# Kernel tuning notes

Hardware: AMD Instinct MI355X
Metric: run time of the kernel (lower is better)

Reference implementation:

```python
import jax, jax.numpy as jnp
import numpy as np

# Architecture constants pinned by the source script
D_MODEL = 2      # input_size / problemDim
ED = 64          # d_inner = expand_factor * d_model = hidden_size
N = 32           # d_state
K = 16           # d_conv
DT_RANK = 1      # ceil(d_model / 16)
NC = 4           # num_classes
B, L = 16, 2048


def setup_inputs() -> dict:
    key = jax.random.key(0)
    ks = jax.random.split(key, 16)
    rn = lambda k, shape, sc=0.1: jax.random.normal(k, shape, jnp.float32) * sc
    return {
        "x": jax.random.normal(ks[0], (B, L, D_MODEL), jnp.float32),
        "norm_w": jnp.ones((D_MODEL,), jnp.float32),
        "w_in": rn(ks[1], (D_MODEL, 2 * ED)),            # in_proj (no bias)
        "conv_w": rn(ks[2], (ED, 1, K)),                  # depthwise causal conv
        "conv_b": rn(ks[3], (ED,)),
        "w_xproj": rn(ks[4], (ED, DT_RANK + 2 * N)),      # x_proj (no bias)
        "w_dt": rn(ks[5], (DT_RANK, ED)),                 # dt_proj
        "b_dt": rn(ks[6], (ED,)),
        "A_log": jnp.log(jnp.tile(jnp.arange(1, N + 1, dtype=jnp.float32), (ED, 1))),
        "D_skip": jnp.ones((ED,), jnp.float32),
        "w_out": rn(ks[7], (ED, ED)),                     # out_proj (classifier mode: d_inner->d_inner)
        "b_out": rn(ks[8], (ED,)),
        "w_fc": rn(ks[9], (ED, ED)),
        "b_fc": rn(ks[10], (ED,)),
        "w_cls": rn(ks[11], (ED, NC)),
        "b_cls": rn(ks[12], (NC,)),
        "w_reg": rn(ks[13], (ED, 1)),
        "b_reg": rn(ks[14], (1,)),
    }


def _rmsnorm(x, w, eps=1e-5):
    return x * jax.lax.rsqrt(jnp.mean(x * x, axis=-1, keepdims=True) + eps) * w


def _silu(x):
    return x * jax.nn.sigmoid(x)


def reference(x, norm_w, w_in, conv_w, conv_b, w_xproj, w_dt, b_dt, A_log, D_skip,
              w_out, b_out, w_fc, b_fc, w_cls, b_cls, w_reg, b_reg):
    # --- Mamba block (n_layers = 1, classifier mode: no residual back to d_model) ---
    h = _rmsnorm(x, norm_w)                                # [B,L,D]
    xz = h @ w_in                                          # [B,L,2*ED]
    xb, z = jnp.split(xz, 2, axis=-1)
    # depthwise causal conv over time (torch pads K-1 both sides then slices [:L] == left-pad K-1)
    xc = jnp.transpose(xb, (0, 2, 1))                      # [B,ED,L]
    xc = jax.lax.conv_general_dilated(
        xc, conv_w, window_strides=(1,), padding=[(K - 1, 0)],
        feature_group_count=ED, dimension_numbers=("NCH", "OIH", "NCH"))
    xc = xc + conv_b[None, :, None]
    xb = _silu(jnp.transpose(xc, (0, 2, 1)))               # [B,L,ED]
    # input-dependent SSM parameters
    dbc = xb @ w_xproj                                     # [B,L,dt_rank+2N]
    delta = jax.nn.softplus(dbc[..., :DT_RANK] @ w_dt + b_dt)   # [B,L,ED]
    Bm = dbc[..., DT_RANK:DT_RANK + N]                     # [B,L,N]
    C = dbc[..., DT_RANK + N:]                             # [B,L,N]
    A = -jnp.exp(A_log)                                    # [ED,N]
    dA = jnp.exp(delta[..., None] * A)                     # [B,L,ED,N]
    dBx = delta[..., None] * Bm[:, :, None, :] * xb[..., None]  # [B,L,ED,N]

    # selective scan: h_t = dA_t * h_{t-1} + dBx_t ; y_t = <h_t, C_t>
    def step(hst, inp):
        dA_t, dBx_t, C_t = inp
        hst = dA_t * hst + dBx_t                           # [B,ED,N]
        y = jnp.einsum("ben,bn->be", hst, C_t)
        return hst, y

    h0 = jnp.zeros((x.shape[0], ED, N), x.dtype)
    xs = (jnp.transpose(dA, (1, 0, 2, 3)),
          jnp.transpose(dBx, (1, 0, 2, 3)),
          jnp.transpose(C, (1, 0, 2)))
    _, ys = jax.lax.scan(step, h0, xs)                     # [L,B,ED]
    y = jnp.transpose(ys, (1, 0, 2)) + D_skip * xb         # [B,L,ED]
    y = y * _silu(z)                                       # gate
    out = y @ w_out + b_out                                # [B,L,ED]

    last = out[:, -1, :]                                   # [B,ED]
    hs = jax.nn.relu(last @ w_fc + b_fc)
    class_logits = hs @ w_cls + b_cls                      # [B,NC]
    mass_pred = (hs @ w_reg + b_reg)[:, 0]                 # [B]
    return class_logits, mass_pred
```

## Files before the change

kernel.cpp:

```cpp
#include <hip/hip_runtime.h>
#include <math.h>

#define BB 16
#define LL 2048
#define ED 64
#define NN 32
#define KK 16
#define NCHUNK 32
#define CH 64
#define NBLK (BB * NCHUNK)

struct ShB {
    float dl[CH][ED];
    float rl[CH][ED];
    float bml[CH][NN + 1];
    float dtr[CH];
};

__global__ __launch_bounds__(256) void k1_featscan(
    const float* __restrict__ x, const float* __restrict__ norm_w,
    const float* __restrict__ w_in, const float* __restrict__ conv_w,
    const float* __restrict__ conv_b, const float* __restrict__ w_xproj,
    const float* __restrict__ w_dt, const float* __restrict__ b_dt,
    const float* __restrict__ A_log,
    float* __restrict__ pbuf, float* __restrict__ sbuf,
    float* __restrict__ xlast, float* __restrict__ zl, float* __restrict__ cl)
{
    const int bx = blockIdx.x;
    const int b = bx >> 5, ti = bx & 31;
    const int l0 = ti * CH;
    const int tid = threadIdx.x;

    __shared__ float xbl[CH][ED + 1];
    __shared__ union { float pre[CH + KK - 1][ED]; ShB sb; } u;
    __shared__ float hh[2 * (CH + KK - 1)];

    if (tid < 2 * (CH + KK - 1)) {
        int p = tid >> 1, c = tid & 1;
        int l = l0 - (KK - 1) + p;
        hh[tid] = (l >= 0) ? x[(b * LL + l) * 2 + c] : 0.f;
    }
    __syncthreads();
    if (tid < CH + KK - 1) {
        float x0 = hh[2 * tid], x1 = hh[2 * tid + 1];
        float s = rsqrtf(0.5f * (x0 * x0 + x1 * x1) + 1e-5f);
        hh[2 * tid]     = x0 * s * norm_w[0];
        hh[2 * tid + 1] = x1 * s * norm_w[1];
    }
    __syncthreads();
    {
        const int e = tid & 63;
        const float w0 = w_in[e], w1 = w_in[128 + e];
        for (int idx = tid; idx < (CH + KK - 1) * ED; idx += 256) {
            int p = idx >> 6;
            u.pre[p][e] = hh[2 * p] * w0 + hh[2 * p + 1] * w1;
        }
    }
    __syncthreads();
    {
        const int e = tid & 63, tg = tid >> 6, t0 = tg * 16;
        float cw[KK];
        #pragma unroll
        for (int k = 0; k < KK; ++k) cw[k] = conv_w[e * KK + k];
        float w[31];
        #pragma unroll
        for (int i = 0; i < 31; ++i) w[i] = u.pre[t0 + i][e];
        const float bias = conv_b[e];
        #pragma unroll
        for (int i = 0; i < 16; ++i) {
            float acc = bias;
            #pragma unroll
            for (int k = 0; k < KK; ++k) acc = __fmaf_rn(cw[k], w[i + k], acc);
            xbl[t0 + i][e] = acc / (1.f + __expf(-acc));
        }
    }
    __syncthreads();

    {
        const int t = tid & 63, jg = tid >> 6;
        const int jstart = (jg == 0) ? 0 : 1 + jg * 8;
        const int jcount = (jg == 0) ? 9 : 8;
        float acc[9];
        #pragma unroll
        for (int jj = 0; jj < 9; ++jj) acc[jj] = 0.f;
        for (int e = 0; e < ED; ++e) {
            float xv = xbl[t][e];
            #pragma unroll
            for (int jj = 0; jj < 9; ++jj)
                if (jj < jcount)
                    acc[jj] = __fmaf_rn(xv, w_xproj[e * 65 + jstart + jj], acc[jj]);
        }
        if (jg == 0) {
            u.sb.dtr[t] = acc[0];
            #pragma unroll
            for (int jj = 1; jj < 9; ++jj) u.sb.bml[t][jj - 1] = acc[jj];
        } else {
            #pragma unroll
            for (int jj = 0; jj < 8; ++jj) u.sb.bml[t][jstart + jj - 1] = acc[jj];
        }
    }
    if (ti == NCHUNK - 1) {
        if (tid < NN) {
            float acc = 0.f;
            for (int e = 0; e < ED; ++e)
                acc = __fmaf_rn(xbl[CH - 1][e], w_xproj[e * 65 + 33 + tid], acc);
            cl[b * NN + tid] = acc;
        } else if (tid >= 64 && tid < 128) {
            int e = tid - 64;
            zl[b * ED + e] = hh[2 * 78] * w_in[64 + e] + hh[2 * 78 + 1] * w_in[192 + e];
        } else if (tid >= 128 && tid < 192) {
            int e = tid - 128;
            xlast[b * ED + e] = xbl[CH - 1][e];
        }
    }
    __syncthreads();

    for (int idx = tid; idx < CH * ED; idx += 256) {
        int s = idx >> 6, e = idx & 63;
        float v = __fmaf_rn(u.sb.dtr[s], w_dt[e], b_dt[e]);
        float d = (v > 15.f) ? v : log1pf(__expf(v));
        u.sb.dl[s][e] = d;
        u.sb.rl[s][e] = __expf(-d);
    }
    __syncthreads();

    {
        const int e = tid & 63, ng = tid >> 6, n0 = ng * 8;
        float S[8];
        #pragma unroll
        for (int j = 0; j < 8; ++j) S[j] = 0.f;
        float Dsum = 0.f;

        for (int s = 0; s < CH; ++s) {
            float d  = u.sb.dl[s][e];
            float xv = xbl[s][e];
            float r  = u.sb.rl[s][e];
            Dsum += d;
            float dx = d * xv;
            float r2 = r * r, r3 = r2 * r, r4 = r2 * r2;
            float r5 = r4 * r, r6 = r3 * r3, r7 = r4 * r3, r8 = r4 * r4;
            float b1 = (ng & 1) ? r8 : 1.f;
            float b2 = (ng & 2) ? r8 * r8 : 1.f;
            float a = r * b1 * b2;
            float pw[8] = {1.f, r, r2, r3, r4, r5, r6, r7};
            #pragma unroll
            for (int j = 0; j < 8; ++j) {
                float dA = a * pw[j];
                S[j] = __fmaf_rn(dA, S[j], dx * u.sb.bml[s][n0 + j]);
            }
        }

        const int gbase = (ti * BB + b) * (ED * NN);
        #pragma unroll
        for (int j = 0; j < 8; ++j) {
            float A = -__expf(A_log[e * NN + n0 + j]);
            int g = gbase + (n0 + j) * ED + e;
            pbuf[g] = __expf(A * Dsum);
            sbuf[g] = S[j];
        }
    }
}

__global__ __launch_bounds__(512) void k2_tail(
    const float* __restrict__ pbuf, const float* __restrict__ sbuf,
    const float* __restrict__ cl, const float* __restrict__ zl,
    const float* __restrict__ xlast, const float* __restrict__ D_skip,
    const float* __restrict__ w_out, const float* __restrict__ b_out,
    const float* __restrict__ w_fc, const float* __restrict__ b_fc,
    const float* __restrict__ w_cls, const float* __restrict__ b_cls,
    const float* __restrict__ w_reg, const float* __restrict__ b_reg,
    float* __restrict__ out)
{
    const int b = blockIdx.x, tid = threadIdx.x;
    const int e = tid & 63, ng = tid >> 6;

    __shared__ float part[8][ED];
    __shared__ float ylds[ED], olds[ED], hlds[ED];

    float h[4] = {0.f, 0.f, 0.f, 0.f};
    for (int c = 0; c < NCHUNK; ++c) {
        int base = (c * BB + b) * (ED * NN);
        #pragma unroll
        for (int s = 0; s < 4; ++s) {
            int g = base + s * 512 + tid;
            h[s] = __fmaf_rn(pbuf[g], h[s], sbuf[g]);
        }
    }
    float acc = 0.f;
    #pragma unroll
    for (int s = 0; s < 4; ++s)
        acc = __fmaf_rn(h[s], cl[b * NN + s * 8 + ng], acc);
    part[ng][e] = acc;
    __syncthreads();

    if (tid < ED) {
        float y = 0.f;
        #pragma unroll
        for (int g = 0; g < 8; ++g) y += part[g][tid];
        y = __fmaf_rn(D_skip[tid], xlast[b * ED + tid], y);
        float z = zl[b * ED + tid];
        y *= z / (1.f + __expf(-z));
        ylds[tid] = y;
    }
    __syncthreads();

    if (tid < ED) {
        float a2 = b_out[tid];
        #pragma unroll 8
        for (int ee = 0; ee < ED; ++ee)
            a2 = __fmaf_rn(ylds[ee], w_out[ee * ED + tid], a2);
        olds[tid] = a2;
    }
    __syncthreads();

    if (tid < ED) {
        float a3 = b_fc[tid];
        #pragma unroll 8
        for (int ee = 0; ee < ED; ++ee)
            a3 = __fmaf_rn(olds[ee], w_fc[ee * ED + tid], a3);
        hlds[tid] = fmaxf(a3, 0.f);
    }
    __syncthreads();

    if (tid < 4) {
        float a4 = b_cls[tid];
        for (int ee = 0; ee < ED; ++ee)
            a4 = __fmaf_rn(hlds[ee], w_cls[ee * 4 + tid], a4);
        out[b * 4 + tid] = a4;
    } else if (tid == 4) {
        float a5 = b_reg[0];
        for (int ee = 0; ee < ED; ++ee)
            a5 = __fmaf_rn(hlds[ee], w_reg[ee], a5);
        out[BB * 4 + b] = a5;
    }
}

extern "C" void kernel_launch(void* const* d_in, const int* in_sizes, int n_in,
                              void* d_out, int out_size, void* d_ws, size_t ws_size,
                              hipStream_t stream) {
    const float* x       = (const float*)d_in[0];
    const float* norm_w  = (const float*)d_in[1];
    const float* w_in    = (const float*)d_in[2];
    const float* conv_w  = (const float*)d_in[3];
    const float* conv_b  = (const float*)d_in[4];
    const float* w_xproj = (const float*)d_in[5];
    const float* w_dt    = (const float*)d_in[6];
    const float* b_dt    = (const float*)d_in[7];
    const float* A_log   = (const float*)d_in[8];
    const float* D_skip  = (const float*)d_in[9];
    const float* w_out   = (const float*)d_in[10];
    const float* b_out   = (const float*)d_in[11];
    const float* w_fc    = (const float*)d_in[12];
    const float* b_fc    = (const float*)d_in[13];
    const float* w_cls   = (const float*)d_in[14];
    const float* b_cls   = (const float*)d_in[15];
    const float* w_reg   = (const float*)d_in[16];
    const float* b_reg   = (const float*)d_in[17];
    float* out = (float*)d_out;

    float* ws    = (float*)d_ws;
    float* pbuf  = ws;
    float* sbuf  = pbuf + NCHUNK * BB * ED * NN;
    float* xlast = sbuf + NCHUNK * BB * ED * NN;
    float* zl    = xlast + BB * ED;
    float* cl    = zl + BB * ED;

    k1_featscan<<<NBLK, 256, 0, stream>>>(x, norm_w, w_in, conv_w, conv_b,
                                          w_xproj, w_dt, b_dt, A_log,
                                          pbuf, sbuf, xlast, zl, cl);
    k2_tail<<<BB, 512, 0, stream>>>(pbuf, sbuf, cl, zl, xlast, D_skip,
                                    w_out, b_out, w_fc, b_fc,
                                    w_cls, b_cls, w_reg, b_reg, out);
}
```

Baseline: 144.4 us.

## Halve chunk size, split chunk fold into wide kernel, drop decay buffer

Doubles the number of time chunks (64 chunks of 32 steps), so the per-block sequential scan is shorter and more blocks are launched. Instead of writing a per-state decay product buffer, each block stores only the per-channel delta sum. A new wide kernel recomputes the decay from A_log and folds all chunks for every (batch, state, channel) element. The x_proj weights are staged in shared memory with float4 reads, dt is computed separately, and softplus uses fast log. This trades an extra kernel launch and more chunk traffic for higher parallelism in both the scan and the cross-chunk fold, which previously ran on only 16 blocks.

```diff
diff --git a/kernel.cpp b/kernel.cpp
--- a/kernel.cpp
+++ b/kernel.cpp
@@ -6,8 +6,8 @@
 #define ED 64
 #define NN 32
 #define KK 16
-#define NCHUNK 32
-#define CH 64
+#define NCHUNK 64
+#define CH 32
 #define NBLK (BB * NCHUNK)
 
 struct ShB {
@@ -22,18 +22,22 @@
     const float* __restrict__ w_in, const float* __restrict__ conv_w,
     const float* __restrict__ conv_b, const float* __restrict__ w_xproj,
     const float* __restrict__ w_dt, const float* __restrict__ b_dt,
-    const float* __restrict__ A_log,
-    float* __restrict__ pbuf, float* __restrict__ sbuf,
+    float* __restrict__ sbuf, float* __restrict__ dsumbuf,
     float* __restrict__ xlast, float* __restrict__ zl, float* __restrict__ cl)
 {
     const int bx = blockIdx.x;
-    const int b = bx >> 5, ti = bx & 31;
+    const int b = bx >> 6, ti = bx & 63;
     const int l0 = ti * CH;
     const int tid = threadIdx.x;
 
     __shared__ float xbl[CH][ED + 1];
-    __shared__ union { float pre[CH + KK - 1][ED]; ShB sb; } u;
     __shared__ float hh[2 * (CH + KK - 1)];
+    __shared__ float wdt[ED];
+    __shared__ __align__(16) union U {
+        float pre[CH + KK - 1][ED];
+        float wx[ED][NN];
+        ShB sb;
+    } u;
 
     if (tid < 2 * (CH + KK - 1)) {
         int p = tid >> 1, c = tid & 1;
@@ -58,16 +62,16 @@
     }
     __syncthreads();
     {
-        const int e = tid & 63, tg = tid >> 6, t0 = tg * 16;
+        const int e = tid & 63, tg = tid >> 6, t0 = tg * 8;
         float cw[KK];
         #pragma unroll
         for (int k = 0; k < KK; ++k) cw[k] = conv_w[e * KK + k];
-        float w[31];
-        #pragma unroll
-        for (int i = 0; i < 31; ++i) w[i] = u.pre[t0 + i][e];
+        float w[8 + KK - 1];
+        #pragma unroll
+        for (int i = 0; i < 8 + KK - 1; ++i) w[i] = u.pre[t0 + i][e];
         const float bias = conv_b[e];
         #pragma unroll
-        for (int i = 0; i < 16; ++i) {
+        for (int i = 0; i < 8; ++i) {
             float acc = bias;
             #pragma unroll
             for (int k = 0; k < KK; ++k) acc = __fmaf_rn(cw[k], w[i + k], acc);
@@ -75,29 +79,33 @@
         }
     }
     __syncthreads();
-
-    {
-        const int t = tid & 63, jg = tid >> 6;
-        const int jstart = (jg == 0) ? 0 : 1 + jg * 8;
-        const int jcount = (jg == 0) ? 9 : 8;
-        float acc[9];
-        #pragma unroll
-        for (int jj = 0; jj < 9; ++jj) acc[jj] = 0.f;
+    for (int idx = tid; idx < ED * NN; idx += 256) {
+        int e = idx >> 5, j = idx & 31;
+        u.wx[e][j] = w_xproj[e * 65 + 1 + j];
+    }
+    if (tid < ED) wdt[tid] = w_xproj[tid * 65];
+    __syncthreads();
+    {
+        const int t = tid & 31, jg = tid >> 5;
+        float a0 = 0.f, a1 = 0.f, a2 = 0.f, a3 = 0.f;
         for (int e = 0; e < ED; ++e) {
             float xv = xbl[t][e];
-            #pragma unroll
-            for (int jj = 0; jj < 9; ++jj)
-                if (jj < jcount)
-                    acc[jj] = __fmaf_rn(xv, w_xproj[e * 65 + jstart + jj], acc[jj]);
-        }
-        if (jg == 0) {
-            u.sb.dtr[t] = acc[0];
-            #pragma unroll
-            for (int jj = 1; jj < 9; ++jj) u.sb.bml[t][jj - 1] = acc[jj];
-        } else {
-            #pragma unroll
-            for (int jj = 0; jj < 8; ++jj) u.sb.bml[t][jstart + jj - 1] = acc[jj];
-        }
+            const float4 wv = *(const float4*)&u.wx[e][jg * 4];
+            a0 = __fmaf_rn(xv, wv.x, a0);
+            a1 = __fmaf_rn(xv, wv.y, a1);
+            a2 = __fmaf_rn(xv, wv.z, a2);
+            a3 = __fmaf_rn(xv, wv.w, a3);
+        }
+        u.sb.bml[t][jg * 4 + 0] = a0;
+        u.sb.bml[t][jg * 4 + 1] = a1;
+        u.sb.bml[t][jg * 4 + 2] = a2;
+        u.sb.bml[t][jg * 4 + 3] = a3;
+    }
+    if (tid < CH) {
+        float acc = 0.f;
+        for (int e = 0; e < ED; ++e)
+            acc = __fmaf_rn(xbl[tid][e], wdt[e], acc);
+        u.sb.dtr[tid] = acc;
     }
     if (ti == NCHUNK - 1) {
         if (tid < NN) {
@@ -107,23 +115,22 @@
             cl[b * NN + tid] = acc;
         } else if (tid >= 64 && tid < 128) {
             int e = tid - 64;
-            zl[b * ED + e] = hh[2 * 78] * w_in[64 + e] + hh[2 * 78 + 1] * w_in[192 + e];
+            int pl = 2 * (CH + KK - 2);
+            zl[b * ED + e] = hh[pl] * w_in[64 + e] + hh[pl + 1] * w_in[192 + e];
         } else if (tid >= 128 && tid < 192) {
             int e = tid - 128;
             xlast[b * ED + e] = xbl[CH - 1][e];
         }
     }
     __syncthreads();
-
     for (int idx = tid; idx < CH * ED; idx += 256) {
         int s = idx >> 6, e = idx & 63;
         float v = __fmaf_rn(u.sb.dtr[s], w_dt[e], b_dt[e]);
-        float d = (v > 15.f) ? v : log1pf(__expf(v));
+        float d = (v > 15.f) ? v : __logf(1.f + __expf(v));
         u.sb.dl[s][e] = d;
         u.sb.rl[s][e] = __expf(-d);
     }
     __syncthreads();
-
     {
         const int e = tid & 63, ng = tid >> 6, n0 = ng * 8;
         float S[8];
@@ -144,59 +151,61 @@
             float a = r * b1 * b2;
             float pw[8] = {1.f, r, r2, r3, r4, r5, r6, r7};
             #pragma unroll
-            for (int j = 0; j < 8; ++j) {
-                float dA = a * pw[j];
-                S[j] = __fmaf_rn(dA, S[j], dx * u.sb.bml[s][n0 + j]);
-            }
+            for (int j = 0; j < 8; ++j)
+                S[j] = __fmaf_rn(a * pw[j], S[j], dx * u.sb.bml[s][n0 + j]);
         }
 
         const int gbase = (ti * BB + b) * (ED * NN);
         #pragma unroll
-        for (int j = 0; j < 8; ++j) {
-            float A = -__expf(A_log[e * NN + n0 + j]);
-            int g = gbase + (n0 + j) * ED + e;
-            pbuf[g] = __expf(A * Dsum);
-            sbuf[g] = S[j];
-        }
-    }
-}
-
-__global__ __launch_bounds__(512) void k2_tail(
-    const float* __restrict__ pbuf, const float* __restrict__ sbuf,
-    const float* __restrict__ cl, const float* __restrict__ zl,
-    const float* __restrict__ xlast, const float* __restrict__ D_skip,
-    const float* __restrict__ w_out, const float* __restrict__ b_out,
-    const float* __restrict__ w_fc, const float* __restrict__ b_fc,
-    const float* __restrict__ w_cls, const float* __restrict__ b_cls,
-    const float* __restrict__ w_reg, const float* __restrict__ b_reg,
-    float* __restrict__ out)
+        for (int j = 0; j < 8; ++j)
+            sbuf[gbase + (n0 + j) * ED + e] = S[j];
+        if (ng == 0) dsumbuf[(ti * BB + b) * ED + e] = Dsum;
+    }
+}
+
+__global__ __launch_bounds__(128) void k2_fold(
+    const float* __restrict__ sbuf, const float* __restrict__ dsumbuf,
+    const float* __restrict__ A_log, float* __restrict__ hfin)
+{
+    const int idx = blockIdx.x * 128 + threadIdx.x;
+    const int b = idx >> 11, r = idx & 2047;
+    const int n = r >> 6, e = r & 63;
+    const float A = -__expf(A_log[e * NN + n]);
+
+    float h = 0.f;
+    for (int c = 0; c < NCHUNK; ++c) {
+        float Ds = dsumbuf[(c * BB + b) * ED + e];
+        float S  = sbuf[(c * BB + b) * (ED * NN) + r];
+        h = __fmaf_rn(__expf(A * Ds), h, S);
+    }
+    hfin[idx] = h;
+}
+
+__global__ __launch_bounds__(256) void k3_tail(
+    const float* __restrict__ hfin, const float* __restrict__ cl,
+    const float* __restrict__ zl, const float* __restrict__ xlast,
+    const float* __restrict__ D_skip, const float* __restrict__ w_out,
+    const float* __restrict__ b_out, const float* __restrict__ w_fc,
+    const float* __restrict__ b_fc, const float* __restrict__ w_cls,
+    const float* __restrict__ b_cls, const float* __restrict__ w_reg,
+    const float* __restrict__ b_reg, float* __restrict__ out)
 {
     const int b = blockIdx.x, tid = threadIdx.x;
-    const int e = tid & 63, ng = tid >> 6;
-
-    __shared__ float part[8][ED];
+    const int e = tid & 63, ng = tid >> 6, n0 = ng * 8;
+
+    __shared__ float part[4][ED];
     __shared__ float ylds[ED], olds[ED], hlds[ED];
 
-    float h[4] = {0.f, 0.f, 0.f, 0.f};
-    for (int c = 0; c < NCHUNK; ++c) {
-        int base = (c * BB + b) * (ED * NN);
-        #pragma unroll
-        for (int s = 0; s < 4; ++s) {
-            int g = base + s * 512 + tid;
-            h[s] = __fmaf_rn(pbuf[g], h[s], sbuf[g]);
-        }
-    }
     float acc = 0.f;
     #pragma unroll
-    for (int s = 0; s < 4; ++s)
-        acc = __fmaf_rn(h[s], cl[b * NN + s * 8 + ng], acc);
+    for (int j = 0; j < 8; ++j)
+        acc = __fmaf_rn(hfin[b * (ED * NN) + (n0 + j) * ED + e],
+                        cl[b * NN + n0 + j], acc);
     part[ng][e] = acc;
     __syncthreads();
 
     if (tid < ED) {
-        float y = 0.f;
-        #pragma unroll
-        for (int g = 0; g < 8; ++g) y += part[g][tid];
+        float y = part[0][tid] + part[1][tid] + part[2][tid] + part[3][tid];
         y = __fmaf_rn(D_skip[tid], xlast[b * ED + tid], y);
         float z = zl[b * ED + tid];
         y *= z / (1.f + __expf(-z));
@@ -258,17 +267,19 @@
     const float* b_reg   = (const float*)d_in[17];
     float* out = (float*)d_out;
 
-    float* ws    = (float*)d_ws;
-    float* pbuf  = ws;
-    float* sbuf  = pbuf + NCHUNK * BB * ED * NN;
-    float* xlast = sbuf + NCHUNK * BB * ED * NN;
-    float* zl    = xlast + BB * ED;
-    float* cl    = zl + BB * ED;
+    float* ws      = (float*)d_ws;
+    float* sbuf    = ws;
+    float* dsumbuf = sbuf + NCHUNK * BB * ED * NN;
+    float* hfin    = dsumbuf + NCHUNK * BB * ED;
+    float* xlast   = hfin + BB * ED * NN;
+    float* zl      = xlast + BB * ED;
+    float* cl      = zl + BB * ED;
 
     k1_featscan<<<NBLK, 256, 0, stream>>>(x, norm_w, w_in, conv_w, conv_b,
-                                          w_xproj, w_dt, b_dt, A_log,
-                                          pbuf, sbuf, xlast, zl, cl);
-    k2_tail<<<BB, 512, 0, stream>>>(pbuf, sbuf, cl, zl, xlast, D_skip,
+                                          w_xproj, w_dt, b_dt,
+                                          sbuf, dsumbuf, xlast, zl, cl);
+    k2_fold<<<(BB * ED * NN) / 128, 128, 0, stream>>>(sbuf, dsumbuf, A_log, hfin);
+    k3_tail<<<BB, 256, 0, stream>>>(hfin, cl, zl, xlast, D_skip,
                                     w_out, b_out, w_fc, b_fc,
                                     w_cls, b_cls, w_reg, b_reg, out);
 }
```

Measured after the change: 121.0 us. -16.2%, faster.
